# Kernel optimization log

Measured on AMD Instinct MI355X. Metric: run time of the kernel, lower is better.

The kernel has to match this reference:

```python
import jax, jax.numpy as jnp
import numpy as np

B, L, H, VOCAB, OUT = 1024, 64, 64, 32000, 5


def setup_inputs() -> dict:
    key = jax.random.key(0)
    k0, k1, k2, k3, k4, k5 = jax.random.split(key, 6)
    leaf_ids = jax.random.randint(k0, (B, L), 0, VOCAB, dtype=jnp.int32)
    embed = jax.random.normal(k1, (VOCAB, H), dtype=jnp.float32) * 0.02
    Vt = jax.random.normal(k2, (H, 2 * H, 2 * H), dtype=jnp.float32) * (1.0 / (2 * H))
    W = jax.random.normal(k3, (2 * H, H), dtype=jnp.float32) * (1.0 / jnp.sqrt(2.0 * H))
    b = jax.random.normal(k4, (1, H), dtype=jnp.float32) * 0.01
    W_out = jax.random.normal(k5, (H, OUT), dtype=jnp.float32) * 0.1
    return {"leaf_ids": leaf_ids, "embed": embed, "Vt": Vt, "W": W, "b": b, "W_out": W_out}


def reference(leaf_ids, embed, Vt, W, b, W_out):
    # Complete binary trees: leaves at depth 0, combine adjacent pairs per level.
    h = embed.shape[1]
    cur = embed[leaf_ids]                         # [B, L, h] leaf embeddings
    all_nodes = [cur.reshape(-1, h)]
    while cur.shape[1] > 1:
        left, right = cur[:, 0::2], cur[:, 1::2]  # [B, n/2, h] each
        stack = jnp.concatenate([left, right], axis=-1)  # [B, n/2, 2h]
        # RNTN bilinear: out_k = s @ V_k @ s^T, batched over all same-level nodes.
        bil = jnp.einsum('bnc,kcd,bnd->bnk', stack, Vt, stack)
        Wx = jnp.einsum('bnc,ch->bnh', stack, W)
        cur = jnp.tanh(bil + Wx + b)              # [B, n/2, h]
        all_nodes.append(cur.reshape(-1, h))
    nodes = jnp.concatenate(all_nodes, axis=0)    # [B*(2L-1), h] (level order)
    return jax.nn.log_softmax(nodes @ W_out, axis=1)
```

## Files before the change

### kernel.cpp

```cpp
#include <hip/hip_runtime.h>
#include <hip/hip_bf16.h>

#define BB 1024

typedef __attribute__((ext_vector_type(8))) short bf16x8;
typedef __attribute__((ext_vector_type(4))) float f32x4;

__device__ __forceinline__ float bf2f(unsigned int u) {
    union { unsigned int i; float f; } v; v.i = u << 16; return v.f;
}
__device__ __forceinline__ float bflo(unsigned int w) {
    union { unsigned int i; float f; } v; v.i = w << 16; return v.f;
}
__device__ __forceinline__ float bfhi(unsigned int w) {
    union { unsigned int i; float f; } v; v.i = w & 0xffff0000u; return v.f;
}
__device__ __forceinline__ unsigned short f2bf(float f) {
    union { float f; unsigned int i; } v; v.f = f;
    return (unsigned short)((v.i + 0x7fffu + ((v.i >> 16) & 1u)) >> 16);
}

__device__ __forceinline__ float gsum(float x) {
    union { float f; int i; } a; a.f = x;
    union { int i; float f; } b;
    b.i = __builtin_amdgcn_ds_swizzle(a.i, 0x401F);
    float s = x + b.f;
    float p0 = s, p1 = s;
    asm("v_permlane32_swap_b32 %0, %1" : "+v"(p0), "+v"(p1));
    return p0 + p1;
}

__global__ __launch_bounds__(256) void prep_kernel(
    const float* __restrict__ Vt, const float* __restrict__ W,
    char* __restrict__ VtB, unsigned short* __restrict__ WT)
{
    const int t = threadIdx.x;
    const int blk = blockIdx.x;
    if (blk < 64) {
        __shared__ float tile[64][132];
        const float* src = Vt + (size_t)blk * 16384;
        for (int h = 0; h < 2; ++h) {
            __syncthreads();
            for (int i = 0; i < 8; ++i) {
                int f4 = t + i * 256;
                int cl = f4 >> 5;
                int d4 = (f4 & 31) << 2;
                const float* s4 = src + (size_t)(h * 64 + cl) * 128 + d4;
                float4 v = *(const float4*)s4;
                tile[cl][d4] = v.x; tile[cl][d4 + 1] = v.y;
                tile[cl][d4 + 2] = v.z; tile[cl][d4 + 3] = v.w;
            }
            __syncthreads();
            int d = t >> 1, ch = t & 1;
            for (int cb = h * 8 + ch * 4; cb < h * 8 + ch * 4 + 4; ++cb) {
                int cbl = cb - h * 8;
                unsigned int w[4];
                #pragma unroll
                for (int j = 0; j < 4; ++j) {
                    unsigned int lo = f2bf(tile[cbl * 8 + 2 * j][d]);
                    unsigned int hi = f2bf(tile[cbl * 8 + 2 * j + 1][d]);
                    w[j] = lo | (hi << 16);
                }
                int oblk = cb ^ (d & 15);
                *(uint4*)(VtB + (size_t)blk * 32768 + d * 256 + oblk * 16) =
                    make_uint4(w[0], w[1], w[2], w[3]);
            }
        }
    } else {
        for (int i = 0; i < 32; ++i) {
            int idx = t * 32 + i;
            int k = idx >> 7, c = idx & 127;
            WT[idx] = f2bf(W[c * 64 + k]);
        }
    }
}

__global__ __launch_bounds__(256) void gather_kernel(
    const int* __restrict__ ids, const float* __restrict__ embed,
    unsigned short* __restrict__ nodes)
{
    int e = blockIdx.x * 256 + threadIdx.x;
    int row = e >> 3;
    int part = e & 7;
    int id = ids[row];
    const float* src = embed + (size_t)id * 64 + part * 8;
    float4 a = *(const float4*)src;
    float4 b = *(const float4*)(src + 4);
    unsigned int w0 = (unsigned int)f2bf(a.x) | ((unsigned int)f2bf(a.y) << 16);
    unsigned int w1 = (unsigned int)f2bf(a.z) | ((unsigned int)f2bf(a.w) << 16);
    unsigned int w2 = (unsigned int)f2bf(b.x) | ((unsigned int)f2bf(b.y) << 16);
    unsigned int w3 = (unsigned int)f2bf(b.z) | ((unsigned int)f2bf(b.w) << 16);
    *(uint4*)(nodes + (size_t)row * 64 + part * 8) = make_uint4(w0, w1, w2, w3);
}

template<int KG>
__global__ __launch_bounds__(512, 1) void bil_kernel(
    unsigned short* __restrict__ nodes, const char* __restrict__ VtB,
    const unsigned short* __restrict__ WT, const float* __restrict__ bias,
    long prev_off, long out_off)
{
    extern __shared__ char smem[];
    float* Y = (float*)smem;

    const int t    = threadIdx.x;
    const int wave = t >> 6;
    const int lane = t & 63;
    const int q    = lane & 15;
    const int g    = lane >> 4;
    const int p    = wave & 1;
    const int dq   = wave >> 1;
    const int k0   = blockIdx.y * KG;
    const long nbase = (long)blockIdx.x * 128;

    const char* prevb = (const char*)(nodes + prev_off * 64);

    uint4 af[4][4];
    uint2 xfp[4][2];
    #pragma unroll
    for (int nb = 0; nb < 4; ++nb) {
        const char* xr = prevb + (nbase + p * 64 + nb * 16 + q) * 256;
        #pragma unroll
        for (int s = 0; s < 4; ++s)
            af[nb][s] = *(const uint4*)(xr + s * 64 + g * 16);
        #pragma unroll
        for (int db = 0; db < 2; ++db)
            xfp[nb][db] = *(const uint2*)(xr + (dq * 32 + db * 16 + g * 4) * 2);
    }

    float yreg[16];
    #pragma unroll
    for (int i = 0; i < 16; ++i) yreg[i] = 0.f;

    {
        const char* src = VtB + (size_t)k0 * 32768 + wave * 4096;
        char* dst = smem + wave * 4096;
        #pragma unroll
        for (int i = 0; i < 4; ++i)
            __builtin_amdgcn_global_load_lds(
                (const unsigned int*)(src + i * 1024 + lane * 16),
                (unsigned int*)(dst + i * 1024 + lane * 16), 16, 0, 0);
    }
    asm volatile("s_waitcnt vmcnt(0)" ::: "memory");
    __syncthreads();

    #pragma unroll
    for (int kk = 0; kk < KG; ++kk) {
        const char* rb = smem + (kk & 1) * 32768;

        if (kk + 1 < KG) {
            const char* src = VtB + (size_t)(k0 + kk + 1) * 32768 + wave * 4096;
            char* dst = smem + ((kk & 1) ^ 1) * 32768 + wave * 4096;
            #pragma unroll
            for (int i = 0; i < 4; ++i)
                __builtin_amdgcn_global_load_lds(
                    (const unsigned int*)(src + i * 1024 + lane * 16),
                    (unsigned int*)(dst + i * 1024 + lane * 16), 16, 0, 0);
        }

        float red[4];
        #pragma unroll
        for (int nb = 0; nb < 4; ++nb) red[nb] = 0.f;

        #pragma unroll
        for (int db = 0; db < 2; ++db) {
            bf16x8 vf[4];
            #pragma unroll
            for (int s = 0; s < 4; ++s)
                vf[s] = *(const bf16x8*)(rb + (dq * 32 + db * 16 + q) * 256
                                         + (((s * 4 + g) ^ q) * 16));
            f32x4 acc[4];
            #pragma unroll
            for (int nb = 0; nb < 4; ++nb) acc[nb] = (f32x4){0.f, 0.f, 0.f, 0.f};
            #pragma unroll
            for (int s = 0; s < 4; ++s)
                #pragma unroll
                for (int nb = 0; nb < 4; ++nb)
                    acc[nb] = __builtin_amdgcn_mfma_f32_16x16x32_bf16(
                        vf[s], *(const bf16x8*)&af[nb][s], acc[nb], 0, 0, 0);
            #pragma unroll
            for (int nb = 0; nb < 4; ++nb) {
                uint2 w = xfp[nb][db];
                red[nb] += acc[nb][0] * bflo(w.x) + acc[nb][1] * bfhi(w.x)
                         + acc[nb][2] * bflo(w.y) + acc[nb][3] * bfhi(w.y);
            }
        }

        #pragma unroll
        for (int nb = 0; nb < 4; ++nb) {
            float v = gsum(red[nb]);
            if (g == (kk >> 2)) yreg[nb * 4 + (kk & 3)] = v;
        }

        asm volatile("s_waitcnt vmcnt(0)" ::: "memory");
        __syncthreads();
    }

    if (dq == 0) {
        f32x4 accw[4];
        #pragma unroll
        for (int nb = 0; nb < 4; ++nb) accw[nb] = (f32x4){0.f, 0.f, 0.f, 0.f};
        #pragma unroll
        for (int s = 0; s < 4; ++s) {
            bf16x8 wtf = *(const bf16x8*)((const char*)WT
                           + (k0 + (q & (KG - 1))) * 256 + s * 64 + g * 16);
            #pragma unroll
            for (int nb = 0; nb < 4; ++nb)
                accw[nb] = __builtin_amdgcn_mfma_f32_16x16x32_bf16(
                    wtf, *(const bf16x8*)&af[nb][s], accw[nb], 0, 0, 0);
        }
        #pragma unroll
        for (int nb = 0; nb < 4; ++nb)
            #pragma unroll
            for (int r = 0; r < 4; ++r)
                yreg[nb * 4 + r] += accw[nb][r];
    }

    #pragma unroll
    for (int nb = 0; nb < 4; ++nb) {
        float4 tmp = make_float4(yreg[nb * 4], yreg[nb * 4 + 1],
                                 yreg[nb * 4 + 2], yreg[nb * 4 + 3]);
        *(float4*)&Y[(wave * 64 + nb * 16 + q) * 20 + g * 4] = tmp;
    }
    __syncthreads();

    constexpr int KQB = KG / 4;
    if (t < 128 * KQB) {
        int n  = t / KQB;
        int kq = t % KQB;
        int pp = n >> 6, nl = n & 63;
        float a0 = 0.f, a1 = 0.f, a2 = 0.f, a3 = 0.f;
        #pragma unroll
        for (int d4 = 0; d4 < 4; ++d4) {
            float4 v = *(const float4*)&Y[((d4 * 2 + pp) * 64 + nl) * 20 + kq * 4];
            a0 += v.x; a1 += v.y; a2 += v.z; a3 += v.w;
        }
        int kb = k0 + kq * 4;
        a0 += bias[kb + 0]; a1 += bias[kb + 1];
        a2 += bias[kb + 2]; a3 += bias[kb + 3];
        unsigned int w0 = (unsigned int)f2bf(tanhf(a0))
                        | ((unsigned int)f2bf(tanhf(a1)) << 16);
        unsigned int w1 = (unsigned int)f2bf(tanhf(a2))
                        | ((unsigned int)f2bf(tanhf(a3)) << 16);
        unsigned short* outp = nodes + out_off * 64;
        *(uint2*)(outp + (nbase + n) * 64 + kb) = make_uint2(w0, w1);
    }
}

__global__ __launch_bounds__(256) void out_kernel(
    const unsigned short* __restrict__ nodes, const float* __restrict__ Wout,
    float* __restrict__ out, int total)
{
    int r = blockIdx.x * 256 + threadIdx.x;
    if (r >= total) return;
    const uint4* xp = (const uint4*)(nodes + (size_t)r * 64);
    float acc[5] = {0.f, 0.f, 0.f, 0.f, 0.f};
    #pragma unroll
    for (int u4 = 0; u4 < 8; ++u4) {
        uint4 v = xp[u4];
        unsigned int ws[4] = {v.x, v.y, v.z, v.w};
        #pragma unroll
        for (int j = 0; j < 4; ++j) {
            int h = u4 * 8 + j * 2;
            float x0 = bf2f(ws[j] & 0xffffu);
            float x1 = bf2f(ws[j] >> 16);
            #pragma unroll
            for (int o = 0; o < 5; ++o) {
                acc[o] = fmaf(x0, Wout[h * 5 + o], acc[o]);
                acc[o] = fmaf(x1, Wout[(h + 1) * 5 + o], acc[o]);
            }
        }
    }
    float m = acc[0];
    #pragma unroll
    for (int o = 1; o < 5; ++o) m = fmaxf(m, acc[o]);
    float s = 0.f;
    #pragma unroll
    for (int o = 0; o < 5; ++o) s += expf(acc[o] - m);
    float ls = logf(s);
    #pragma unroll
    for (int o = 0; o < 5; ++o) out[(size_t)r * 5 + o] = acc[o] - m - ls;
}

extern "C" void kernel_launch(void* const* d_in, const int* in_sizes, int n_in,
                              void* d_out, int out_size, void* d_ws, size_t ws_size,
                              hipStream_t stream) {
    const int*   ids   = (const int*)d_in[0];
    const float* embed = (const float*)d_in[1];
    const float* Vt    = (const float*)d_in[2];
    const float* W     = (const float*)d_in[3];
    const float* bias  = (const float*)d_in[4];
    const float* Wout  = (const float*)d_in[5];
    float* out = (float*)d_out;

    char* ws = (char*)d_ws;
    unsigned short* nodes = (unsigned short*)ws;
    char* VtB = ws + 16646144;
    unsigned short* WT = (unsigned short*)(ws + 18743296);

    prep_kernel<<<65, 256, 0, stream>>>(Vt, W, VtB, WT);
    gather_kernel<<<2048, 256, 0, stream>>>(ids, embed, nodes);

    (void)hipFuncSetAttribute(reinterpret_cast<const void*>(bil_kernel<16>),
                              hipFuncAttributeMaxDynamicSharedMemorySize, 65536);
    (void)hipFuncSetAttribute(reinterpret_cast<const void*>(bil_kernel<8>),
                              hipFuncAttributeMaxDynamicSharedMemorySize, 65536);
    (void)hipFuncSetAttribute(reinterpret_cast<const void*>(bil_kernel<4>),
                              hipFuncAttributeMaxDynamicSharedMemorySize, 65536);

    const int kgs[6] = {16, 16, 16, 8, 4, 4};
    long off_prev = 0, off_cur = 65536;
    int n = 32;
    for (int lev = 0; lev < 6; ++lev) {
        long M = (long)BB * n;
        int kg = kgs[lev];
        dim3 grid((unsigned)(M / 128), (unsigned)(64 / kg));
        if (kg == 16)
            bil_kernel<16><<<grid, 512, 65536, stream>>>(nodes, VtB, WT, bias,
                                                         off_prev, off_cur);
        else if (kg == 8)
            bil_kernel<8><<<grid, 512, 65536, stream>>>(nodes, VtB, WT, bias,
                                                        off_prev, off_cur);
        else
            bil_kernel<4><<<grid, 512, 65536, stream>>>(nodes, VtB, WT, bias,
                                                        off_prev, off_cur);
        off_prev = off_cur; off_cur += M; n >>= 1;
    }
    out_kernel<<<(130048 + 255) / 256, 256, 0, stream>>>(nodes, Wout, out, 130048);
}
```

Measured before the change: 202.8 us.

## Restructure bilinear kernel: per-wave private Vt buffers, 64-node blocks, no per-k barriers

The bilinear kernel now gives each of the 8 waves its own 16-row slice of V_k, double-buffered in a private LDS region, so the per-k __syncthreads is removed. Each block covers 64 nodes instead of 128, which doubles the grid. Launch bounds now allow 4 blocks per SM, and the level KG schedule is adjusted. The group reduction uses permlane16_swap instead of ds_swizzle, and the cross-wave reduction now sums 8 partials. In exchange, Vt traffic per node doubles and each block holds 64KB of dynamic LDS, which may limit occupancy.

Result: slower. 555.0 us (+173.7%).

```diff
diff --git a/kernel.cpp b/kernel.cpp
--- a/kernel.cpp
+++ b/kernel.cpp
@@ -21,13 +21,12 @@
 }
 
 __device__ __forceinline__ float gsum(float x) {
-    union { float f; int i; } a; a.f = x;
-    union { int i; float f; } b;
-    b.i = __builtin_amdgcn_ds_swizzle(a.i, 0x401F);
-    float s = x + b.f;
-    float p0 = s, p1 = s;
-    asm("v_permlane32_swap_b32 %0, %1" : "+v"(p0), "+v"(p1));
-    return p0 + p1;
+    float a0 = x, a1 = x;
+    asm("v_permlane16_swap_b32 %0, %1" : "+v"(a0), "+v"(a1));
+    float s = a0 + a1;
+    float b0 = s, b1 = s;
+    asm("v_permlane32_swap_b32 %0, %1" : "+v"(b0), "+v"(b1));
+    return b0 + b1;
 }
 
 __global__ __launch_bounds__(256) void prep_kernel(
@@ -94,7 +93,7 @@
 }
 
 template<int KG>
-__global__ __launch_bounds__(512, 1) void bil_kernel(
+__global__ __launch_bounds__(512, 4) void bil_kernel(
     unsigned short* __restrict__ nodes, const char* __restrict__ VtB,
     const unsigned short* __restrict__ WT, const float* __restrict__ bias,
     long prev_off, long out_off)
@@ -107,49 +106,50 @@
     const int lane = t & 63;
     const int q    = lane & 15;
     const int g    = lane >> 4;
-    const int p    = wave & 1;
-    const int dq   = wave >> 1;
     const int k0   = blockIdx.y * KG;
-    const long nbase = (long)blockIdx.x * 128;
+    const long nbase = (long)blockIdx.x * 64;
 
     const char* prevb = (const char*)(nodes + prev_off * 64);
 
     uint4 af[4][4];
-    uint2 xfp[4][2];
+    float xf[4][4];
     #pragma unroll
     for (int nb = 0; nb < 4; ++nb) {
-        const char* xr = prevb + (nbase + p * 64 + nb * 16 + q) * 256;
+        const char* xr = prevb + (nbase + nb * 16 + q) * 256;
         #pragma unroll
         for (int s = 0; s < 4; ++s)
             af[nb][s] = *(const uint4*)(xr + s * 64 + g * 16);
-        #pragma unroll
-        for (int db = 0; db < 2; ++db)
-            xfp[nb][db] = *(const uint2*)(xr + (dq * 32 + db * 16 + g * 4) * 2);
+        uint2 v = *(const uint2*)(xr + (wave * 16 + g * 4) * 2);
+        xf[nb][0] = bflo(v.x); xf[nb][1] = bfhi(v.x);
+        xf[nb][2] = bflo(v.y); xf[nb][3] = bfhi(v.y);
     }
 
     float yreg[16];
     #pragma unroll
     for (int i = 0; i < 16; ++i) yreg[i] = 0.f;
 
-    {
-        const char* src = VtB + (size_t)k0 * 32768 + wave * 4096;
-        char* dst = smem + wave * 4096;
-        #pragma unroll
-        for (int i = 0; i < 4; ++i)
-            __builtin_amdgcn_global_load_lds(
-                (const unsigned int*)(src + i * 1024 + lane * 16),
-                (unsigned int*)(dst + i * 1024 + lane * 16), 16, 0, 0);
-    }
+    char* mybuf = smem + wave * 8192;
+    const char* ksrc = VtB + (size_t)k0 * 32768 + wave * 4096;
+
+    #pragma unroll
+    for (int i = 0; i < 4; ++i)
+        __builtin_amdgcn_global_load_lds(
+            (const unsigned int*)(ksrc + i * 1024 + lane * 16),
+            (unsigned int*)(mybuf + i * 1024 + lane * 16), 16, 0, 0);
     asm volatile("s_waitcnt vmcnt(0)" ::: "memory");
-    __syncthreads();
 
     #pragma unroll
     for (int kk = 0; kk < KG; ++kk) {
-        const char* rb = smem + (kk & 1) * 32768;
+        const char* rb = mybuf + (kk & 1) * 4096;
+
+        bf16x8 vf[4];
+        #pragma unroll
+        for (int s = 0; s < 4; ++s)
+            vf[s] = *(const bf16x8*)(rb + q * 256 + (((s * 4 + g) ^ q) * 16));
 
         if (kk + 1 < KG) {
-            const char* src = VtB + (size_t)(k0 + kk + 1) * 32768 + wave * 4096;
-            char* dst = smem + ((kk & 1) ^ 1) * 32768 + wave * 4096;
+            const char* src = ksrc + (size_t)(kk + 1) * 32768;
+            char* dst = mybuf + ((kk & 1) ^ 1) * 4096;
             #pragma unroll
             for (int i = 0; i < 4; ++i)
                 __builtin_amdgcn_global_load_lds(
@@ -157,45 +157,29 @@
                     (unsigned int*)(dst + i * 1024 + lane * 16), 16, 0, 0);
         }
 
-        float red[4];
-        #pragma unroll
-        for (int nb = 0; nb < 4; ++nb) red[nb] = 0.f;
-
-        #pragma unroll
-        for (int db = 0; db < 2; ++db) {
-            bf16x8 vf[4];
-            #pragma unroll
-            for (int s = 0; s < 4; ++s)
-                vf[s] = *(const bf16x8*)(rb + (dq * 32 + db * 16 + q) * 256
-                                         + (((s * 4 + g) ^ q) * 16));
-            f32x4 acc[4];
-            #pragma unroll
-            for (int nb = 0; nb < 4; ++nb) acc[nb] = (f32x4){0.f, 0.f, 0.f, 0.f};
-            #pragma unroll
-            for (int s = 0; s < 4; ++s)
-                #pragma unroll
-                for (int nb = 0; nb < 4; ++nb)
-                    acc[nb] = __builtin_amdgcn_mfma_f32_16x16x32_bf16(
-                        vf[s], *(const bf16x8*)&af[nb][s], acc[nb], 0, 0, 0);
-            #pragma unroll
-            for (int nb = 0; nb < 4; ++nb) {
-                uint2 w = xfp[nb][db];
-                red[nb] += acc[nb][0] * bflo(w.x) + acc[nb][1] * bfhi(w.x)
-                         + acc[nb][2] * bflo(w.y) + acc[nb][3] * bfhi(w.y);
-            }
-        }
+        f32x4 acc[4];
+        #pragma unroll
+        for (int nb = 0; nb < 4; ++nb) acc[nb] = (f32x4){0.f, 0.f, 0.f, 0.f};
+        #pragma unroll
+        for (int s = 0; s < 4; ++s)
+            #pragma unroll
+            for (int nb = 0; nb < 4; ++nb)
+                acc[nb] = __builtin_amdgcn_mfma_f32_16x16x32_bf16(
+                    vf[s], *(const bf16x8*)&af[nb][s], acc[nb], 0, 0, 0);
 
         #pragma unroll
         for (int nb = 0; nb < 4; ++nb) {
-            float v = gsum(red[nb]);
+            float red = acc[nb][0] * xf[nb][0] + acc[nb][1] * xf[nb][1]
+                      + acc[nb][2] * xf[nb][2] + acc[nb][3] * xf[nb][3];
+            float v = gsum(red);
             if (g == (kk >> 2)) yreg[nb * 4 + (kk & 3)] = v;
         }
 
-        asm volatile("s_waitcnt vmcnt(0)" ::: "memory");
-        __syncthreads();
-    }
-
-    if (dq == 0) {
+        if (kk + 1 < KG)
+            asm volatile("s_waitcnt vmcnt(0)" ::: "memory");
+    }
+
+    if (wave == 0) {
         f32x4 accw[4];
         #pragma unroll
         for (int nb = 0; nb < 4; ++nb) accw[nb] = (f32x4){0.f, 0.f, 0.f, 0.f};
@@ -214,6 +198,8 @@
             for (int r = 0; r < 4; ++r)
                 yreg[nb * 4 + r] += accw[nb][r];
     }
+
+    __syncthreads();
 
     #pragma unroll
     for (int nb = 0; nb < 4; ++nb) {
@@ -224,14 +210,13 @@
     __syncthreads();
 
     constexpr int KQB = KG / 4;
-    if (t < 128 * KQB) {
+    if (t < 64 * KQB) {
         int n  = t / KQB;
         int kq = t % KQB;
-        int pp = n >> 6, nl = n & 63;
         float a0 = 0.f, a1 = 0.f, a2 = 0.f, a3 = 0.f;
         #pragma unroll
-        for (int d4 = 0; d4 < 4; ++d4) {
-            float4 v = *(const float4*)&Y[((d4 * 2 + pp) * 64 + nl) * 20 + kq * 4];
+        for (int w = 0; w < 8; ++w) {
+            float4 v = *(const float4*)&Y[(w * 64 + n) * 20 + kq * 4];
             a0 += v.x; a1 += v.y; a2 += v.z; a3 += v.w;
         }
         int kb = k0 + kq * 4;
@@ -307,13 +292,13 @@
     (void)hipFuncSetAttribute(reinterpret_cast<const void*>(bil_kernel<4>),
                               hipFuncAttributeMaxDynamicSharedMemorySize, 65536);
 
-    const int kgs[6] = {16, 16, 16, 8, 4, 4};
+    const int kgs[6] = {16, 16, 16, 16, 8, 4};
     long off_prev = 0, off_cur = 65536;
     int n = 32;
     for (int lev = 0; lev < 6; ++lev) {
         long M = (long)BB * n;
         int kg = kgs[lev];
-        dim3 grid((unsigned)(M / 128), (unsigned)(64 / kg));
+        dim3 grid((unsigned)(M / 64), (unsigned)(64 / kg));
         if (kg == 16)
             bil_kernel<16><<<grid, 512, 65536, stream>>>(nodes, VtB, WT, bias,
                                                          off_prev, off_cur);
```
